# Optimization experiments

Measured on AMD Instinct MI355X. Metric: run time of the kernel, lower is better.

## Reference

```python
import jax, jax.numpy as jnp
import numpy as np

B, T, C, H = 4, 2048, 1024, 16
D = C // H  # head dim = 64


def setup_inputs() -> dict:
    key = jax.random.key(0)
    k_x, k_wa, k_ba, k_wp, k_bp = jax.random.split(key, 5)
    s = 1.0 / np.sqrt(C)
    return {
        "x": jax.random.normal(k_x, (B, T, C), dtype=jnp.float32),
        "w_attn": jax.random.uniform(k_wa, (C, 3 * C), minval=-s, maxval=s, dtype=jnp.float32),
        "b_attn": jax.random.uniform(k_ba, (3 * C,), minval=-s, maxval=s, dtype=jnp.float32),
        "w_proj": jax.random.uniform(k_wp, (C, C), minval=-s, maxval=s, dtype=jnp.float32),
        "b_proj": jax.random.uniform(k_bp, (C,), minval=-s, maxval=s, dtype=jnp.float32),
    }


def reference(x, w_attn, b_attn, w_proj, b_proj):
    b, t, c = x.shape
    qkv = x @ w_attn + b_attn  # [b, t, 3c]
    q, k, v = jnp.split(qkv, 3, axis=-1)
    # [b, h, t, d]
    q = q.reshape(b, t, H, D).transpose(0, 2, 1, 3)
    k = k.reshape(b, t, H, D).transpose(0, 2, 1, 3)
    v = v.reshape(b, t, H, D).transpose(0, 2, 1, 3)
    scale = 1.0 / np.sqrt(D)
    logits = jnp.einsum("bhqd,bhkd->bhqk", q, k) * scale
    causal = jnp.tril(jnp.ones((t, t), dtype=bool))
    logits = jnp.where(causal, logits, jnp.finfo(logits.dtype).min)
    attn = jax.nn.softmax(logits, axis=-1)
    y = jnp.einsum("bhqk,bhkd->bhqd", attn, v)
    y = y.transpose(0, 2, 1, 3).reshape(b, t, c)
    return y @ w_proj + b_proj
```

## Files before the change

### kernel.cpp

```cpp
#include <hip/hip_runtime.h>


using u16 = unsigned short;
using u32 = unsigned int;
using bf16x8 = __attribute__((ext_vector_type(8))) __bf16;
using f32x4  = __attribute__((ext_vector_type(4))) float;
using f32x16 = __attribute__((ext_vector_type(16))) float;
using u16x8  = __attribute__((ext_vector_type(8))) u16;
using u16x4  = __attribute__((ext_vector_type(4))) u16;
using u32x2  = __attribute__((ext_vector_type(2))) u32;
using u32x4  = __attribute__((ext_vector_type(4))) u32;
using fvec4  = __attribute__((ext_vector_type(4))) float;

__device__ __forceinline__ u16 f2bf(float f) {
  u32 u = __builtin_bit_cast(u32, f);
  u32 r = (u + 0x7FFFu + ((u >> 16) & 1u)) >> 16;
  return (u16)r;
}

__device__ __forceinline__ u32 cvtpk(float lo, float hi) {
  u32 r;
  asm("v_cvt_pk_bf16_f32 %0, %1, %2" : "=v"(r) : "v"(lo), "v"(hi));
  return r;
}

__device__ __forceinline__ f32x4 mfma16(bf16x8 a, bf16x8 b, f32x4 c) {
  return __builtin_amdgcn_mfma_f32_16x16x32_bf16(a, b, c, 0, 0, 0);
}

__device__ __forceinline__ f32x16 mfma32(bf16x8 a, bf16x8 b, f32x16 c) {
  return __builtin_amdgcn_mfma_f32_32x32x16_bf16(a, b, c, 0, 0, 0);
}

__device__ __forceinline__ void gld16(const u16* g, u16* l) {
  __builtin_amdgcn_global_load_lds(
      (const __attribute__((address_space(1))) void*)g,
      (__attribute__((address_space(3))) void*)l, 16, 0, 0);
}

__device__ __forceinline__ void lgkm_barrier() {
  asm volatile("s_waitcnt lgkmcnt(0)" ::: "memory");
  __builtin_amdgcn_s_barrier();
  __builtin_amdgcn_sched_barrier(0);
}

__global__ __launch_bounds__(256) void conv_kernel(
    const float* __restrict__ in, u16* __restrict__ out) {
  const size_t i = ((size_t)blockIdx.x * 256 + threadIdx.x) * 8;
  fvec4 a = *(const fvec4*)(in + i);
  fvec4 b = *(const fvec4*)(in + i + 4);
  u16x8 h;
#pragma unroll
  for (int j = 0; j < 4; ++j) { h[j] = f2bf(a[j]); h[4 + j] = f2bf(b[j]); }
  *(u16x8*)(out + i) = h;
}

__global__ __launch_bounds__(256) void transpose_conv_kernel(
    const float* __restrict__ W, u16* __restrict__ Wt, int K, int N) {
  __shared__ float tile[32][33];
  const int n0 = blockIdx.x * 32, k0 = blockIdx.y * 32;
  const int tx = threadIdx.x, ty = threadIdx.y;
#pragma unroll
  for (int j = 0; j < 4; ++j)
    tile[ty + j * 8][tx] = W[(size_t)(k0 + ty + j * 8) * N + n0 + tx];
  __syncthreads();
#pragma unroll
  for (int j = 0; j < 4; ++j)
    Wt[(size_t)(n0 + ty + j * 8) * K + k0 + tx] = f2bf(tile[tx][ty + j * 8]);
}

template <bool QKV>
__global__ __launch_bounds__(256) void gemm_kernel(
    const u16* __restrict__ A, const u16* __restrict__ Bt,
    const float* __restrict__ bias, void* __restrict__ Cp,
    u16* __restrict__ vt, int M, int N, int K) {
  constexpr float SC = 0.18033688011112042f;
  __shared__ u16 As[2][4096];
  __shared__ u16 Bs[2][4096];
  const int tid = threadIdx.x;
  const int l = tid & 63, w = tid >> 6;
  const int l15 = l & 15, l16 = l >> 4;
  const int wm = (w >> 1) * 64, wn = (w & 1) * 64;

  const u32 nwg = gridDim.x * gridDim.y;
  u32 f = blockIdx.y * gridDim.x + blockIdx.x;
  f = (f & 7) * (nwg >> 3) + (f >> 3);
  const long mbase = (long)(f / gridDim.x) * 128;
  const long nbase = (long)(f % gridDim.x) * 128;

  const int srow = tid >> 2;
  const int scol = ((tid & 3) ^ ((srow >> 1) & 3)) * 8;
  const u16* gA0 = A + (mbase + srow) * (long)K + scol;
  const u16* gA1 = gA0 + 64 * (long)K;
  const u16* gB0 = Bt + (nbase + srow) * (long)K + scol;
  const u16* gB1 = gB0 + 64 * (long)K;

  f32x4 acc[4][4] = {};
  const int NT = K >> 5;

#define STAGE(buf, koff)                         \
  gld16(gA0 + (koff), &As[buf][tid * 8]);        \
  gld16(gA1 + (koff), &As[buf][tid * 8 + 2048]); \
  gld16(gB0 + (koff), &Bs[buf][tid * 8]);        \
  gld16(gB1 + (koff), &Bs[buf][tid * 8 + 2048]);

  STAGE(0, 0);
  asm volatile("s_waitcnt vmcnt(0)" ::: "memory");
  __builtin_amdgcn_s_barrier();

  for (int t = 0; t < NT; ++t) {
    const int cur = t & 1;
    if (t + 1 < NT) { STAGE(cur ^ 1, (t + 1) * 32); }

    bf16x8 af[4], bfr[4];
#pragma unroll
    for (int i = 0; i < 4; ++i) {
      const int row = wm + i * 16 + l15;
      af[i] = *(const bf16x8*)(&As[cur][row * 32 + ((l16 ^ ((row >> 1) & 3)) * 8)]);
    }
#pragma unroll
    for (int j = 0; j < 4; ++j) {
      const int row = wn + j * 16 + l15;
      bfr[j] = *(const bf16x8*)(&Bs[cur][row * 32 + ((l16 ^ ((row >> 1) & 3)) * 8)]);
    }
    asm volatile("s_waitcnt lgkmcnt(0)" ::: "memory");
    __builtin_amdgcn_sched_barrier(0);
    __builtin_amdgcn_s_setprio(1);
#pragma unroll
    for (int i = 0; i < 4; ++i)
#pragma unroll
      for (int j = 0; j < 4; ++j)
        acc[i][j] = mfma16(af[i], bfr[j], acc[i][j]);
    __builtin_amdgcn_s_setprio(0);
    __builtin_amdgcn_sched_barrier(0);
    if (t + 1 < NT) { asm volatile("s_waitcnt vmcnt(0)" ::: "memory"); }
    __builtin_amdgcn_s_barrier();
  }
#undef STAGE

  if constexpr (QKV) {
    const bool isv = (nbase >= 2048);
#pragma unroll
    for (int i = 0; i < 4; ++i) {
#pragma unroll
      for (int j = 0; j < 4; ++j) {
        const long m0 = mbase + wm + i * 16 + l16 * 4;
        const int n = (int)nbase + wn + j * 16 + l15;
        const float bv = bias[n];
        if (!isv) {
          u16* qkp = (u16*)Cp;
          const float sc = (n < 1024) ? SC : 1.0f;
#pragma unroll
          for (int r = 0; r < 4; ++r)
            qkp[(m0 + r) * 2048 + n] = f2bf((acc[i][j][r] + bv) * sc);
        } else {
          const int vc = n - 2048, hh = vc >> 6, dd = vc & 63;
          const int bb = (int)(m0 >> 11), t0 = (int)(m0 & 2047);
          u16x4 pk;
#pragma unroll
          for (int r = 0; r < 4; ++r) pk[r] = f2bf(acc[i][j][r] + bv);
          *(u16x4*)(vt + ((size_t)(bb * 16 + hh) * 64 + dd) * 2048 + t0) = pk;
        }
      }
    }
  } else {
#pragma unroll
    for (int i = 0; i < 4; ++i) {
#pragma unroll
      for (int j = 0; j < 4; ++j) {
        const long row0 = mbase + wm + i * 16 + l16 * 4;
        const long col = nbase + wn + j * 16 + l15;
        const float bv = bias[col];
#pragma unroll
        for (int r = 0; r < 4; ++r)
          ((float*)Cp)[(row0 + r) * (long)N + col] = acc[i][j][r] + bv;
      }
    }
  }
}

__global__ __launch_bounds__(256, 2) void flash_kernel(
    const u16* __restrict__ qk, const u16* __restrict__ vt, u16* __restrict__ attn_out) {
  constexpr float MFIX = 4.0f;
  __shared__ u16 Ks[2][64 * 64];
  __shared__ u16 Vs[2][64 * 64];
  const int tid = threadIdx.x;
  const int lane = tid & 63, w = tid >> 6;
  const int l31 = lane & 31, hi = lane >> 5;
  const int xorv = (l31 & 7) << 4;

  const u32 i = blockIdx.y * 8 + blockIdx.x;
  const int jj = i >> 3;
  const int bh = (i & 7) | ((jj & 7) << 3);
  const int pair = (int)(i >> 6);
  const int b = bh >> 4, h = bh & 15;
  const u16* qbase = qk + (size_t)b * 2048 * 2048 + h * 64;
  const u16* kbase = qbase + 1024;
  const u16* vbase = vt + (size_t)bh * 64 * 2048;
  u16* obase = attn_out + (size_t)b * 2048 * 1024 + h * 64;

  const int r0 = tid >> 3, c0 = (tid & 7) * 8;
  const int sco = ((c0 * 2) ^ ((r0 & 7) << 4)) >> 1;

  int cur = 0;
  for (int half = 0; half < 2; ++half) {
    const int qt = half ? (15 - pair) : pair;
    const int nt = 2 * qt + 2;
    const int qr0 = qt * 128 + w * 32;
    const int q = qr0 + l31;

    bf16x8 qf[4];
#pragma unroll
    for (int ds = 0; ds < 4; ++ds)
      qf[ds] = *(const bf16x8*)(qbase + (size_t)q * 2048 + ds * 16 + hi * 8);

    f32x16 oacc[2] = {};
    float lsum = 0.f;

    u16x8 kreg[2], vreg[2];
    kreg[0] = *(const u16x8*)(kbase + (size_t)r0 * 2048 + c0);
    kreg[1] = *(const u16x8*)(kbase + (size_t)(r0 + 32) * 2048 + c0);
    vreg[0] = *(const u16x8*)(vbase + (size_t)r0 * 2048 + c0);
    vreg[1] = *(const u16x8*)(vbase + (size_t)(r0 + 32) * 2048 + c0);

    for (int kt = 0; kt < nt; ++kt) {
      const int kb = kt * 64;
      *(u16x8*)(&Ks[cur][r0 * 64 + sco]) = kreg[0];
      *(u16x8*)(&Ks[cur][(r0 + 32) * 64 + sco]) = kreg[1];
      *(u16x8*)(&Vs[cur][r0 * 64 + sco]) = vreg[0];
      *(u16x8*)(&Vs[cur][(r0 + 32) * 64 + sco]) = vreg[1];
      lgkm_barrier();
      if (kt + 1 < nt) {
        const int nb = kb + 64;
        kreg[0] = *(const u16x8*)(kbase + (size_t)(nb + r0) * 2048 + c0);
        kreg[1] = *(const u16x8*)(kbase + (size_t)(nb + r0 + 32) * 2048 + c0);
        vreg[0] = *(const u16x8*)(vbase + (size_t)r0 * 2048 + nb + c0);
        vreg[1] = *(const u16x8*)(vbase + (size_t)(r0 + 32) * 2048 + nb + c0);
      }

      f32x16 s0 = {}, s1 = {};
      __builtin_amdgcn_s_setprio(1);
#pragma unroll
      for (int ds = 0; ds < 4; ++ds) {
        const int col = (ds * 32 + hi * 16) ^ xorv;
        bf16x8 k0 = *(const bf16x8*)((const char*)&Ks[cur][0] + l31 * 128 + col);
        bf16x8 k1 = *(const bf16x8*)((const char*)&Ks[cur][0] + (32 + l31) * 128 + col);
        s0 = mfma32(k0, qf[ds], s0);
        s1 = mfma32(k1, qf[ds], s1);
      }
      __builtin_amdgcn_s_setprio(0);

      if (kb + 63 > qr0) {
#pragma unroll
        for (int r = 0; r < 16; ++r) {
          const int crow = (r & 3) + 8 * (r >> 2) + 4 * hi;
          if (kb + crow > q) s0[r] = -1e30f;
          if (kb + 32 + crow > q) s1[r] = -1e30f;
        }
      }

      float p0[16], p1[16];
      float ps = 0.f;
#pragma unroll
      for (int r = 0; r < 16; ++r) {
        p0[r] = exp2f(s0[r] - MFIX);
        p1[r] = exp2f(s1[r] - MFIX);
        ps += p0[r] + p1[r];
      }
      lsum += ps;

      bf16x8 pf[4];
#pragma unroll
      for (int kh = 0; kh < 2; ++kh) {
#pragma unroll
        for (int c = 0; c < 2; ++c) {
          const float* pp = kh ? p1 : p0;
          const int bs = c * 8;
          u32 L0 = cvtpk(pp[bs + 0], pp[bs + 1]);
          u32 L1 = cvtpk(pp[bs + 2], pp[bs + 3]);
          u32 L2 = cvtpk(pp[bs + 4], pp[bs + 5]);
          u32 L3 = cvtpk(pp[bs + 6], pp[bs + 7]);
          asm("v_permlane32_swap_b32 %0, %1" : "+v"(L0), "+v"(L2));
          asm("v_permlane32_swap_b32 %0, %1" : "+v"(L1), "+v"(L3));
          u32x4 pk = {L0, L1, L2, L3};
          pf[kh * 2 + c] = __builtin_bit_cast(bf16x8, pk);
        }
      }

      __builtin_amdgcn_s_setprio(1);
#pragma unroll
      for (int dh = 0; dh < 2; ++dh) {
#pragma unroll
        for (int ks = 0; ks < 4; ++ks) {
          const int col = (ks * 32 + hi * 16) ^ xorv;
          bf16x8 vf = *(const bf16x8*)((const char*)&Vs[cur][0] + (dh * 32 + l31) * 128 + col);
          oacc[dh] = mfma32(vf, pf[ks], oacc[dh]);
        }
      }
      __builtin_amdgcn_s_setprio(0);
      cur ^= 1;
    }

    lsum += __shfl_xor(lsum, 32);
    const float inv = 1.0f / lsum;
    u16* orow = obase + (size_t)q * 1024;
#pragma unroll
    for (int dh = 0; dh < 2; ++dh) {
#pragma unroll
      for (int jq = 0; jq < 4; ++jq) {
        u32x2 pk;
        pk[0] = cvtpk(oacc[dh][jq * 4 + 0] * inv, oacc[dh][jq * 4 + 1] * inv);
        pk[1] = cvtpk(oacc[dh][jq * 4 + 2] * inv, oacc[dh][jq * 4 + 3] * inv);
        *(u32x2*)(orow + dh * 32 + 8 * jq + 4 * hi) = pk;
      }
    }
  }
}

extern "C" void kernel_launch(void* const* d_in, const int* in_sizes, int n_in,
                              void* d_out, int out_size, void* d_ws, size_t ws_size,
                              hipStream_t stream) {
  (void)in_sizes; (void)n_in; (void)out_size; (void)ws_size;
  const float* x      = (const float*)d_in[0];
  const float* w_attn = (const float*)d_in[1];
  const float* b_attn = (const float*)d_in[2];
  const float* w_proj = (const float*)d_in[3];
  const float* b_proj = (const float*)d_in[4];
  float* out = (float*)d_out;

  char* ws = (char*)d_ws;
  u16* qkbuf = (u16*)(ws);
  u16* vtbuf = (u16*)(ws + 33554432);
  u16* xbf   = (u16*)(ws + 50331648);
  u16* attnb = (u16*)(ws + 50331648);
  u16* wtA   = (u16*)(ws + 67108864);
  u16* wtP   = (u16*)(ws + 73400320);

  conv_kernel<<<4096, 256, 0, stream>>>(x, xbf);
  transpose_conv_kernel<<<dim3(3072 / 32, 1024 / 32), dim3(32, 8), 0, stream>>>(w_attn, wtA, 1024, 3072);
  transpose_conv_kernel<<<dim3(1024 / 32, 1024 / 32), dim3(32, 8), 0, stream>>>(w_proj, wtP, 1024, 1024);

  gemm_kernel<true><<<dim3(3072 / 128, 8192 / 128), 256, 0, stream>>>(
      xbf, wtA, b_attn, qkbuf, vtbuf, 8192, 3072, 1024);

  flash_kernel<<<dim3(8, 64), 256, 0, stream>>>(qkbuf, vtbuf, attnb);

  gemm_kernel<false><<<dim3(1024 / 128, 8192 / 128), 256, 0, stream>>>(
      attnb, wtP, b_proj, out, nullptr, 8192, 1024, 1024);
}
```

Before: 177.9 us.

## Load K via direct global-to-LDS, read V fragments from global, drop LDS staging of V

K tiles are now loaded into LDS with global_load_lds (async direct-to-LDS) using a pre-swizzled source address, double-buffered with a vmcnt wait and barrier at the end of each iteration. V is no longer staged through LDS: each lane loads its MFMA operand fragments straight from global memory. This halves LDS use and removes the register-to-LDS store traffic. The trade-off is uncoalesced, redundant global reads for V, and V latency that sits directly on the PV MFMA path. The fixed exp2 offset MFIX is also dropped, which changes numerical headroom but not the work done.

```diff
diff --git a/kernel.cpp b/kernel.cpp
--- a/kernel.cpp
+++ b/kernel.cpp
@@ -36,12 +36,6 @@
   __builtin_amdgcn_global_load_lds(
       (const __attribute__((address_space(1))) void*)g,
       (__attribute__((address_space(3))) void*)l, 16, 0, 0);
-}
-
-__device__ __forceinline__ void lgkm_barrier() {
-  asm volatile("s_waitcnt lgkmcnt(0)" ::: "memory");
-  __builtin_amdgcn_s_barrier();
-  __builtin_amdgcn_sched_barrier(0);
 }
 
 __global__ __launch_bounds__(256) void conv_kernel(
@@ -181,9 +175,7 @@
 
 __global__ __launch_bounds__(256, 2) void flash_kernel(
     const u16* __restrict__ qk, const u16* __restrict__ vt, u16* __restrict__ attn_out) {
-  constexpr float MFIX = 4.0f;
   __shared__ u16 Ks[2][64 * 64];
-  __shared__ u16 Vs[2][64 * 64];
   const int tid = threadIdx.x;
   const int lane = tid & 63, w = tid >> 6;
   const int l31 = lane & 31, hi = lane >> 5;
@@ -199,8 +191,9 @@
   const u16* vbase = vt + (size_t)bh * 64 * 2048;
   u16* obase = attn_out + (size_t)b * 2048 * 1024 + h * 64;
 
-  const int r0 = tid >> 3, c0 = (tid & 7) * 8;
-  const int sco = ((c0 * 2) ^ ((r0 & 7) << 4)) >> 1;
+  const int srow = tid >> 3;
+  const int sslot = (tid & 7) ^ (srow & 7);
+  const u16* gk = kbase + (size_t)srow * 2048 + sslot * 8;
 
   int cur = 0;
   for (int half = 0; half < 2; ++half) {
@@ -217,26 +210,23 @@
     f32x16 oacc[2] = {};
     float lsum = 0.f;
 
-    u16x8 kreg[2], vreg[2];
-    kreg[0] = *(const u16x8*)(kbase + (size_t)r0 * 2048 + c0);
-    kreg[1] = *(const u16x8*)(kbase + (size_t)(r0 + 32) * 2048 + c0);
-    vreg[0] = *(const u16x8*)(vbase + (size_t)r0 * 2048 + c0);
-    vreg[1] = *(const u16x8*)(vbase + (size_t)(r0 + 32) * 2048 + c0);
+    gld16(gk, &Ks[cur][tid * 8]);
+    gld16(gk + (size_t)32 * 2048, &Ks[cur][tid * 8 + 2048]);
+    asm volatile("s_waitcnt vmcnt(0)" ::: "memory");
+    __builtin_amdgcn_s_barrier();
 
     for (int kt = 0; kt < nt; ++kt) {
       const int kb = kt * 64;
-      *(u16x8*)(&Ks[cur][r0 * 64 + sco]) = kreg[0];
-      *(u16x8*)(&Ks[cur][(r0 + 32) * 64 + sco]) = kreg[1];
-      *(u16x8*)(&Vs[cur][r0 * 64 + sco]) = vreg[0];
-      *(u16x8*)(&Vs[cur][(r0 + 32) * 64 + sco]) = vreg[1];
-      lgkm_barrier();
       if (kt + 1 < nt) {
-        const int nb = kb + 64;
-        kreg[0] = *(const u16x8*)(kbase + (size_t)(nb + r0) * 2048 + c0);
-        kreg[1] = *(const u16x8*)(kbase + (size_t)(nb + r0 + 32) * 2048 + c0);
-        vreg[0] = *(const u16x8*)(vbase + (size_t)r0 * 2048 + nb + c0);
-        vreg[1] = *(const u16x8*)(vbase + (size_t)(r0 + 32) * 2048 + nb + c0);
-      }
+        gld16(gk + (size_t)(kb + 64) * 2048, &Ks[cur ^ 1][tid * 8]);
+        gld16(gk + (size_t)(kb + 96) * 2048, &Ks[cur ^ 1][tid * 8 + 2048]);
+      }
+      u16x8 vf[2][4];
+#pragma unroll
+      for (int dh = 0; dh < 2; ++dh)
+#pragma unroll
+        for (int ks = 0; ks < 4; ++ks)
+          vf[dh][ks] = *(const u16x8*)(vbase + (size_t)(dh * 32 + l31) * 2048 + kb + ks * 16 + hi * 8);
 
       f32x16 s0 = {}, s1 = {};
       __builtin_amdgcn_s_setprio(1);
@@ -263,8 +253,8 @@
       float ps = 0.f;
 #pragma unroll
       for (int r = 0; r < 16; ++r) {
-        p0[r] = exp2f(s0[r] - MFIX);
-        p1[r] = exp2f(s1[r] - MFIX);
+        p0[r] = exp2f(s0[r]);
+        p1[r] = exp2f(s1[r]);
         ps += p0[r] + p1[r];
       }
       lsum += ps;
@@ -289,15 +279,14 @@
 
       __builtin_amdgcn_s_setprio(1);
 #pragma unroll
-      for (int dh = 0; dh < 2; ++dh) {
-#pragma unroll
-        for (int ks = 0; ks < 4; ++ks) {
-          const int col = (ks * 32 + hi * 16) ^ xorv;
-          bf16x8 vf = *(const bf16x8*)((const char*)&Vs[cur][0] + (dh * 32 + l31) * 128 + col);
-          oacc[dh] = mfma32(vf, pf[ks], oacc[dh]);
-        }
-      }
+      for (int dh = 0; dh < 2; ++dh)
+#pragma unroll
+        for (int ks = 0; ks < 4; ++ks)
+          oacc[dh] = mfma32(__builtin_bit_cast(bf16x8, vf[dh][ks]), pf[ks], oacc[dh]);
       __builtin_amdgcn_s_setprio(0);
+
+      asm volatile("s_waitcnt vmcnt(0)" ::: "memory");
+      __builtin_amdgcn_s_barrier();
       cur ^= 1;
     }
 
```

New measurement: 203.4 us. +14.3%, slower.
